# Kernel tuning notes

Measured on AMD Instinct MI355X. Metric: run time of the kernel, lower is better.

The kernel has to match this reference:

```python
import jax, jax.numpy as jnp
import numpy as np

DISTANCES = [1, 2]
ANGLES_DEG = [0.0, 45.0, 90.0, 135.0]
LEVELS = 32
FEATURES = ["contrast", "homogeneity", "energy", "correlation"]

# skimage graycomatrix offsets: row = r + round(sin(a)*d), col = c + round(cos(a)*d)
OFFSETS = [(int(np.round(np.sin(np.deg2rad(a)) * d)), int(np.round(np.cos(np.deg2rad(a)) * d)))
           for d in DISTANCES for a in ANGLES_DEG]


def _quantize(images, levels):
    # RGB -> gray, [-1,1] -> [0,1] -> integer gray levels (uint8 floor cast in original)
    gray = images.mean(axis=1)                                  # [B,H,W]
    g = jnp.clip((gray + 1.0) * 0.5 * (levels - 1), 0.0, levels - 1)
    return g.astype(jnp.int32)


def _glcm(g, dr, dc, levels):
    # symmetric, normed co-occurrence matrix for one (distance, angle) offset
    B, H, W = g.shape
    r0, r1 = max(0, -dr), H - max(0, dr)
    c0, c1 = max(0, -dc), W - max(0, dc)
    i = g[:, r0:r1, c0:c1]
    j = g[:, r0 + dr:r1 + dr, c0 + dc:c1 + dc]
    idx = (i * levels + j).reshape(B, -1)                        # [B, n_pairs]
    hist = jax.vmap(lambda ix: jnp.zeros(levels * levels, jnp.float32).at[ix].add(1.0))(idx)
    P = hist.reshape(B, levels, levels)
    P = P + jnp.swapaxes(P, 1, 2)                                # symmetric
    return P / jnp.sum(P, axis=(1, 2), keepdims=True)            # normed


def _prop(P, feat):
    # graycoprops formulas; P: [B, L, L]
    L = P.shape[-1]
    I = jnp.arange(L, dtype=jnp.float32)[:, None]                # [L,1]
    J = jnp.arange(L, dtype=jnp.float32)[None, :]                # [1,L]
    if feat == "contrast":
        return jnp.sum(P * (I - J) ** 2, axis=(1, 2))
    if feat == "homogeneity":
        return jnp.sum(P / (1.0 + (I - J) ** 2), axis=(1, 2))
    if feat == "energy":
        return jnp.sqrt(jnp.sum(P * P, axis=(1, 2)))
    if feat == "correlation":
        mu_i = jnp.sum(I * P, axis=(1, 2))                       # [B]
        mu_j = jnp.sum(J * P, axis=(1, 2))
        di = I[None] - mu_i[:, None, None]
        dj = J[None] - mu_j[:, None, None]
        std_i = jnp.sqrt(jnp.sum(P * di * di, axis=(1, 2)))
        std_j = jnp.sqrt(jnp.sum(P * dj * dj, axis=(1, 2)))
        cov = jnp.sum(P * di * dj, axis=(1, 2))
        denom = std_i * std_j
        return jnp.where(denom > 1e-15, cov / jnp.where(denom > 1e-15, denom, 1.0), 1.0)
    raise ValueError(feat)


def reference(images):
    g = _quantize(images, LEVELS)
    # accumulate feature values over all (distance, angle) offsets, then mean
    acc = {f: 0.0 for f in FEATURES}
    for (dr, dc) in OFFSETS:
        P = _glcm(g, dr, dc, LEVELS)
        for f in FEATURES:
            acc[f] = acc[f] + _prop(P, f)
    n = float(len(OFFSETS))
    return jnp.stack([acc[f] / n for f in FEATURES], axis=0)     # [n_features, B]


def setup_inputs() -> dict:
    key = jax.random.key(0)
    images = jax.random.normal(key, (64, 3, 512, 512), dtype=jnp.float32)
    return {"images": images}
```

## Files before the change

kernel.cpp:

```cpp
#include <hip/hip_runtime.h>

typedef unsigned int uint;

#define HW (512 * 512)
#define NIMG 64
#define NUQ 6
#define QSTRIDE 528
#define FLB 32768
#define QRB 57344
#define SMEM_BYTES 61568

__device__ __constant__ float UOFF_W[NUQ] = {1.f, 2.f, 1.f, 2.f, 1.f, 1.f};
__device__ __constant__ float NPAIRS[NUQ] = {
    512.f * 511.f, 511.f * 511.f, 511.f * 512.f,
    511.f * 511.f, 512.f * 510.f, 510.f * 512.f};

__device__ __forceinline__ uint q1f(float a, float b, float c) {
    float t = fmaf(a + b + c, 5.1666665f, 15.5f);
    t = fminf(fmaxf(t, 0.0f), 31.0f);
    return (uint)t;
}

__global__ __launch_bounds__(256) void glcm_fused(
    const float* __restrict__ in, uint* __restrict__ wire) {
    __shared__ __align__(16) unsigned char smem[SMEM_BYTES];
    const int tid = threadIdx.x;
    const int b = blockIdx.x >> 4;
    const int s = blockIdx.x & 15;
    const int rs = s * 32;
    const int w = tid >> 6;
    const int lane = tid & 63;
    const float* ib = in + (size_t)b * (3 * HW);

    {
        uint4 z = make_uint4(0, 0, 0, 0);
        #pragma unroll
        for (int q = 0; q < 8; ++q)
            *(uint4*)(smem + tid * 16 + q * 4096) = z;
    }

    auto issue = [&](int cc) {
        const int slot = cc & 1;
        const int R0 = rs - 2 + 2 * cc;
        #pragma unroll
        for (int ch = 0; ch < 3; ++ch) {
            int row = min(max(R0 + (w >> 1), 0), 511);
            const float* src = ib + ch * HW + row * 512 + (w & 1) * 256 + lane * 4;
            __builtin_amdgcn_global_load_lds(
                (const __attribute__((address_space(1))) void*)src,
                (__attribute__((address_space(3))) void*)(smem + FLB + slot * 12288 + (ch * 4 + w) * 1024),
                16, 0, 0);
        }
    };

    issue(0);

    for (int c = 0; c <= 18; ++c) {
        if (c + 1 <= 17) issue(c + 1);

        const int h = c - 2;
        if (h >= 1 && h <= 16) {
            const int lr = tid >> 7;
            const int dq = tid & 127;
            const int R = rs - 2 + 2 * h + lr;
            const unsigned char* qr = smem + QRB;
            const uint* rowL   = (const uint*)(qr + ((R)     & 7) * QSTRIDE);
            const uint* rowLm  = (const uint*)(qr + ((R - 1) & 7) * QSTRIDE);
            const uint* rowLp  = (const uint*)(qr + ((R + 1) & 7) * QSTRIDE);
            const uint* rowLpp = (const uint*)(qr + ((R + 2) & 7) * QSTRIDE);
            uint A = rowL[dq],  A1 = rowL[dq + 1];
            uint B = rowLp[dq], B1 = rowLp[dq + 1];
            uint C = rowLm[dq], C1 = rowLm[dq + 1];
            uint D = rowLpp[dq];

            auto pp4 = [&](uint jw, int tagoff, uint inc, int rlo, int rhi) {
                if (R >= rlo && R < rhi) {
                    uint a0 = __builtin_amdgcn_perm(A, jw, 0x0C0C0400u) & 0xFCFCu;
                    uint a1 = __builtin_amdgcn_perm(A, jw, 0x0C0C0501u) & 0xFCFCu;
                    uint a2 = __builtin_amdgcn_perm(A, jw, 0x0C0C0602u) & 0xFCFCu;
                    uint a3 = __builtin_amdgcn_perm(A, jw, 0x0C0C0703u) & 0xFCFCu;
                    atomicAdd((uint*)(smem + tagoff + a0), inc);
                    atomicAdd((uint*)(smem + tagoff + a1), inc);
                    atomicAdd((uint*)(smem + tagoff + a2), inc);
                    atomicAdd((uint*)(smem + tagoff + a3), inc);
                }
            };
            pp4(__builtin_amdgcn_alignbyte(A1, A, 1), 0,   1u,     0, 512);
            pp4(__builtin_amdgcn_alignbyte(B1, B, 1), 256, 1u,     0, 511);
            pp4(B,                                    512, 1u,     0, 511);
            pp4(__builtin_amdgcn_alignbyte(C1, C, 1), 0,   65536u, 1, 512);
            pp4(__builtin_amdgcn_alignbyte(A1, A, 2), 256, 65536u, 0, 512);
            pp4(D,                                    512, 65536u, 0, 510);
        }

        __syncthreads();

        if (c <= 17) {
            const int r = tid >> 7;
            const int c4 = (tid & 127) << 2;
            const int R = rs - 2 + 2 * c + r;
            const float* fb = (const float*)(smem + FLB + (c & 1) * 12288);
            float4 f0 = *(const float4*)(fb + 0 * 1024 + r * 512 + c4);
            float4 f1 = *(const float4*)(fb + 1 * 1024 + r * 512 + c4);
            float4 f2 = *(const float4*)(fb + 2 * 1024 + r * 512 + c4);
            uint q = (q1f(f0.x, f1.x, f2.x) << 2)
                   | (q1f(f0.y, f1.y, f2.y) << 10)
                   | (q1f(f0.z, f1.z, f2.z) << 18)
                   | (q1f(f0.w, f1.w, f2.w) << 26);
            unsigned char* qrw = smem + QRB + ((R) & 7) * QSTRIDE;
            *(uint*)(qrw + c4) = q;
            if ((tid & 127) == 127)
                *(uint4*)(qrw + 512) =
                    make_uint4(0x80808080u, 0x80808080u, 0x80808080u, 0x80808080u);
        }

        __syncthreads();
    }

    uint* hb = wire + (size_t)blockIdx.x * 3072;
    const uint* hist = (const uint*)smem;
    #pragma unroll
    for (int qq = 0; qq < 12; ++qq) {
        int o = tid + qq * 256;
        int tg = o >> 10, ij = o & 1023;
        int i = ij >> 5, j = ij & 31;
        hb[o] = hist[(i << 8) | (tg << 6) | j];
    }
}

__global__ __launch_bounds__(256) void feature_out_kernel(
    const uint* __restrict__ wire, float* __restrict__ out) {
    const int b = blockIdx.x;
    __shared__ uint cnt[NUQ][1024];
    __shared__ float fred[NUQ][4];
    const int tid = threadIdx.x, wid = tid >> 6, lane = tid & 63;

    for (int u = wid; u < NUQ; u += 4) {
        const int tg = (u < 3) ? u : u - 3;
        const int sh = (u < 3) ? 0 : 16;
        const uint* p = wire + (size_t)b * (16 * 3072) + tg * 1024;
        for (int ij = lane; ij < 1024; ij += 64) {
            uint acc = 0;
            #pragma unroll
            for (int st = 0; st < 16; ++st)
                acc += (p[(size_t)st * 3072 + ij] >> sh) & 0xFFFFu;
            cnt[u][ij] = acc;
        }
    }
    __syncthreads();

    for (int u = wid; u < NUQ; u += 4) {
        const float inv_total = 1.0f / (2.0f * NPAIRS[u]);
        float c_sum = 0, h_sum = 0, e_sum = 0, m1 = 0, m2 = 0, m12 = 0;
        for (int k = lane; k < 1024; k += 64) {
            int i = k >> 5, j = k & 31;
            float sym = (float)(cnt[u][k] + cnt[u][(j << 5) | i]);
            float P = sym * inv_total;
            float d = (float)(i - j);
            float d2 = d * d;
            float fi = (float)i, fj = (float)j;
            c_sum += P * d2;
            h_sum += P / (1.0f + d2);
            e_sum += P * P;
            m1 += P * fi; m2 += P * fi * fi; m12 += P * fi * fj;
        }
        #pragma unroll
        for (int sft = 32; sft > 0; sft >>= 1) {
            c_sum += __shfl_down(c_sum, sft);
            h_sum += __shfl_down(h_sum, sft);
            e_sum += __shfl_down(e_sum, sft);
            m1 += __shfl_down(m1, sft);
            m2 += __shfl_down(m2, sft);
            m12 += __shfl_down(m12, sft);
        }
        if (lane == 0) {
            float mu = m1, var = m2 - mu * mu, cov = m12 - mu * mu;
            float corr = (var > 1e-15f) ? cov / var : 1.0f;
            fred[u][0] = c_sum; fred[u][1] = h_sum;
            fred[u][2] = sqrtf(e_sum); fred[u][3] = corr;
        }
    }
    __syncthreads();
    if (tid < 4) {
        float acc = 0.f;
        #pragma unroll
        for (int u = 0; u < NUQ; ++u) acc += UOFF_W[u] * fred[u][tid];
        out[tid * NIMG + b] = acc * 0.125f;
    }
}

extern "C" void kernel_launch(void* const* d_in, const int* in_sizes, int n_in,
                              void* d_out, int out_size, void* d_ws, size_t ws_size,
                              hipStream_t stream) {
    const float* images = (const float*)d_in[0];
    float* out = (float*)d_out;
    uint* wire = (uint*)d_ws;

    glcm_fused<<<NIMG * 16, 256, 0, stream>>>(images, wire);
    feature_out_kernel<<<NIMG, 256, 0, stream>>>(wire, out);
}
```

Measured before the change: 71.97 us.

## Replace LDS-staged row pipeline with per-thread register row tiles

The GLCM kernel no longer stages float rows into LDS with async loads and double buffering. Each thread now loads a 16-column by 8-row strip directly from global memory, quantizes it into registers, and keeps the previous two quantized rows in registers to form all six offset pairs. This removes the per-row __syncthreads pairs and the LDS staging buffer, and halves the block count to 8 bands per image. In exchange it re-reads halo rows and columns from global memory, uses uncoalesced strided float4 loads, and launches fewer blocks, which may reduce occupancy and latency hiding.

```diff
diff --git a/kernel.cpp b/kernel.cpp
--- a/kernel.cpp
+++ b/kernel.cpp
@@ -5,10 +5,7 @@
 #define HW (512 * 512)
 #define NIMG 64
 #define NUQ 6
-#define QSTRIDE 528
-#define FLB 32768
-#define QRB 57344
-#define SMEM_BYTES 61568
+#define NBAND 8
 
 __device__ __constant__ float UOFF_W[NUQ] = {1.f, 2.f, 1.f, 2.f, 1.f, 1.f};
 __device__ __constant__ float NPAIRS[NUQ] = {
@@ -23,108 +20,94 @@
 
 __global__ __launch_bounds__(256) void glcm_fused(
     const float* __restrict__ in, uint* __restrict__ wire) {
-    __shared__ __align__(16) unsigned char smem[SMEM_BYTES];
+    __shared__ __align__(16) uint hist[8192];
     const int tid = threadIdx.x;
-    const int b = blockIdx.x >> 4;
-    const int s = blockIdx.x & 15;
-    const int rs = s * 32;
-    const int w = tid >> 6;
-    const int lane = tid & 63;
+    const int b = blockIdx.x >> 3;
+    const int band = blockIdx.x & 7;
+    const int cg = tid & 31;
+    const int ts = tid >> 5;
+    const int r0 = band * 64 + ts * 8;
+    const int c0 = cg << 4;
     const float* ib = in + (size_t)b * (3 * HW);
+    unsigned char* hb8 = (unsigned char*)hist;
 
     {
         uint4 z = make_uint4(0, 0, 0, 0);
         #pragma unroll
         for (int q = 0; q < 8; ++q)
-            *(uint4*)(smem + tid * 16 + q * 4096) = z;
+            *(uint4*)(hb8 + tid * 16 + q * 4096) = z;
     }
+    __syncthreads();
 
-    auto issue = [&](int cc) {
-        const int slot = cc & 1;
-        const int R0 = rs - 2 + 2 * cc;
+    auto qrow = [&](int r, uint w[5]) {
+        const float* base = ib + ((size_t)r << 9);
         #pragma unroll
-        for (int ch = 0; ch < 3; ++ch) {
-            int row = min(max(R0 + (w >> 1), 0), 511);
-            const float* src = ib + ch * HW + row * 512 + (w & 1) * 256 + lane * 4;
-            __builtin_amdgcn_global_load_lds(
-                (const __attribute__((address_space(1))) void*)src,
-                (__attribute__((address_space(3))) void*)(smem + FLB + slot * 12288 + (ch * 4 + w) * 1024),
-                16, 0, 0);
+        for (int k = 0; k < 5; ++k) {
+            int cc = (k < 4) ? (c0 + 4 * k) : min(c0 + 16, 508);
+            float4 f0 = *(const float4*)(base + cc);
+            float4 f1 = *(const float4*)(base + HW + cc);
+            float4 f2 = *(const float4*)(base + 2 * HW + cc);
+            w[k] = (q1f(f0.x, f1.x, f2.x) << 2)
+                 | (q1f(f0.y, f1.y, f2.y) << 10)
+                 | (q1f(f0.z, f1.z, f2.z) << 18)
+                 | (q1f(f0.w, f1.w, f2.w) << 26);
         }
+        if (cg == 31) w[4] = 0x80808080u;
     };
 
-    issue(0);
+    auto pp = [&](uint IW, uint JW, int tagoff, uint inc) {
+        uint a0 = __builtin_amdgcn_perm(IW, JW, 0x0C0C0400u) & 0xFCFCu;
+        uint a1 = __builtin_amdgcn_perm(IW, JW, 0x0C0C0501u) & 0xFCFCu;
+        uint a2 = __builtin_amdgcn_perm(IW, JW, 0x0C0C0602u) & 0xFCFCu;
+        uint a3 = __builtin_amdgcn_perm(IW, JW, 0x0C0C0703u) & 0xFCFCu;
+        atomicAdd((uint*)(hb8 + tagoff + a0), inc);
+        atomicAdd((uint*)(hb8 + tagoff + a1), inc);
+        atomicAdd((uint*)(hb8 + tagoff + a2), inc);
+        atomicAdd((uint*)(hb8 + tagoff + a3), inc);
+    };
 
-    for (int c = 0; c <= 18; ++c) {
-        if (c + 1 <= 17) issue(c + 1);
+    uint p2[5] = {0, 0, 0, 0, 0}, p1[5] = {0, 0, 0, 0, 0}, cur[5];
+    if (r0 >= 2) qrow(r0 - 2, p2);
+    if (r0 >= 1) qrow(r0 - 1, p1);
 
-        const int h = c - 2;
-        if (h >= 1 && h <= 16) {
-            const int lr = tid >> 7;
-            const int dq = tid & 127;
-            const int R = rs - 2 + 2 * h + lr;
-            const unsigned char* qr = smem + QRB;
-            const uint* rowL   = (const uint*)(qr + ((R)     & 7) * QSTRIDE);
-            const uint* rowLm  = (const uint*)(qr + ((R - 1) & 7) * QSTRIDE);
-            const uint* rowLp  = (const uint*)(qr + ((R + 1) & 7) * QSTRIDE);
-            const uint* rowLpp = (const uint*)(qr + ((R + 2) & 7) * QSTRIDE);
-            uint A = rowL[dq],  A1 = rowL[dq + 1];
-            uint B = rowLp[dq], B1 = rowLp[dq + 1];
-            uint C = rowLm[dq], C1 = rowLm[dq + 1];
-            uint D = rowLpp[dq];
+    for (int it = 0; it < 8; ++it) {
+        const int r = r0 + it;
+        qrow(r, cur);
 
-            auto pp4 = [&](uint jw, int tagoff, uint inc, int rlo, int rhi) {
-                if (R >= rlo && R < rhi) {
-                    uint a0 = __builtin_amdgcn_perm(A, jw, 0x0C0C0400u) & 0xFCFCu;
-                    uint a1 = __builtin_amdgcn_perm(A, jw, 0x0C0C0501u) & 0xFCFCu;
-                    uint a2 = __builtin_amdgcn_perm(A, jw, 0x0C0C0602u) & 0xFCFCu;
-                    uint a3 = __builtin_amdgcn_perm(A, jw, 0x0C0C0703u) & 0xFCFCu;
-                    atomicAdd((uint*)(smem + tagoff + a0), inc);
-                    atomicAdd((uint*)(smem + tagoff + a1), inc);
-                    atomicAdd((uint*)(smem + tagoff + a2), inc);
-                    atomicAdd((uint*)(smem + tagoff + a3), inc);
-                }
-            };
-            pp4(__builtin_amdgcn_alignbyte(A1, A, 1), 0,   1u,     0, 512);
-            pp4(__builtin_amdgcn_alignbyte(B1, B, 1), 256, 1u,     0, 511);
-            pp4(B,                                    512, 1u,     0, 511);
-            pp4(__builtin_amdgcn_alignbyte(C1, C, 1), 0,   65536u, 1, 512);
-            pp4(__builtin_amdgcn_alignbyte(A1, A, 2), 256, 65536u, 0, 512);
-            pp4(D,                                    512, 65536u, 0, 510);
+        #pragma unroll
+        for (int k = 0; k < 4; ++k) {
+            uint C1 = __builtin_amdgcn_alignbyte(cur[k + 1], cur[k], 1);
+            uint C2 = __builtin_amdgcn_alignbyte(cur[k + 1], cur[k], 2);
+            pp(cur[k], C1, 0,   1u);
+            pp(cur[k], C2, 256, 65536u);
         }
+        if (r >= 1) {
+            #pragma unroll
+            for (int k = 0; k < 4; ++k) {
+                uint C1 = __builtin_amdgcn_alignbyte(cur[k + 1], cur[k], 1);
+                uint P1 = __builtin_amdgcn_alignbyte(p1[k + 1], p1[k], 1);
+                pp(p1[k], cur[k], 512, 1u);
+                pp(p1[k], C1,     256, 1u);
+                pp(cur[k], P1,    0,   65536u);
+            }
+            if (r >= 2) {
+                #pragma unroll
+                for (int k = 0; k < 4; ++k)
+                    pp(p2[k], cur[k], 512, 65536u);
+            }
+        }
+        #pragma unroll
+        for (int k = 0; k < 5; ++k) { p2[k] = p1[k]; p1[k] = cur[k]; }
+    }
+    __syncthreads();
 
-        __syncthreads();
-
-        if (c <= 17) {
-            const int r = tid >> 7;
-            const int c4 = (tid & 127) << 2;
-            const int R = rs - 2 + 2 * c + r;
-            const float* fb = (const float*)(smem + FLB + (c & 1) * 12288);
-            float4 f0 = *(const float4*)(fb + 0 * 1024 + r * 512 + c4);
-            float4 f1 = *(const float4*)(fb + 1 * 1024 + r * 512 + c4);
-            float4 f2 = *(const float4*)(fb + 2 * 1024 + r * 512 + c4);
-            uint q = (q1f(f0.x, f1.x, f2.x) << 2)
-                   | (q1f(f0.y, f1.y, f2.y) << 10)
-                   | (q1f(f0.z, f1.z, f2.z) << 18)
-                   | (q1f(f0.w, f1.w, f2.w) << 26);
-            unsigned char* qrw = smem + QRB + ((R) & 7) * QSTRIDE;
-            *(uint*)(qrw + c4) = q;
-            if ((tid & 127) == 127)
-                *(uint4*)(qrw + 512) =
-                    make_uint4(0x80808080u, 0x80808080u, 0x80808080u, 0x80808080u);
-        }
-
-        __syncthreads();
-    }
-
-    uint* hb = wire + (size_t)blockIdx.x * 3072;
-    const uint* hist = (const uint*)smem;
+    uint* hw = wire + (size_t)blockIdx.x * 3072;
     #pragma unroll
     for (int qq = 0; qq < 12; ++qq) {
         int o = tid + qq * 256;
         int tg = o >> 10, ij = o & 1023;
         int i = ij >> 5, j = ij & 31;
-        hb[o] = hist[(i << 8) | (tg << 6) | j];
+        hw[o] = hist[(i << 8) | (tg << 6) | j];
     }
 }
 
@@ -138,11 +121,11 @@
     for (int u = wid; u < NUQ; u += 4) {
         const int tg = (u < 3) ? u : u - 3;
         const int sh = (u < 3) ? 0 : 16;
-        const uint* p = wire + (size_t)b * (16 * 3072) + tg * 1024;
+        const uint* p = wire + (size_t)b * (NBAND * 3072) + tg * 1024;
         for (int ij = lane; ij < 1024; ij += 64) {
             uint acc = 0;
             #pragma unroll
-            for (int st = 0; st < 16; ++st)
+            for (int st = 0; st < NBAND; ++st)
                 acc += (p[(size_t)st * 3072 + ij] >> sh) & 0xFFFFu;
             cnt[u][ij] = acc;
         }
@@ -196,6 +179,6 @@
     float* out = (float*)d_out;
     uint* wire = (uint*)d_ws;
 
-    glcm_fused<<<NIMG * 16, 256, 0, stream>>>(images, wire);
+    glcm_fused<<<NIMG * NBAND, 256, 0, stream>>>(images, wire);
     feature_out_kernel<<<NIMG, 256, 0, stream>>>(wire, out);
 }
```

After: 81.46 us. 13.2% more time.
